# Optimization experiments

Hardware: AMD Instinct MI355X
Metric: run time of the kernel (lower is better)

## Reference

```python
import jax, jax.numpy as jnp
import numpy as np

MUL = 8              # multiplicity of 0e and 1o irreps (feature dim = MUL + 3*MUL = 32)
N_NODES = 25000
N_EDGES = 200000
EDGE_ATTR_DIM = 16
RADIAL_HIDDEN = 64
N_PATHS = 5          # CG paths: 0e*0e->0e, 0e*1o->1o, 1o*0e->1o, 1o*1o->0e, 1o*1o->1o


def _split(x):
    # x: [*, MUL + 3*MUL] -> scalars [*, MUL], vectors [*, MUL, 3]
    return x[:, :MUL], x[:, MUL:].reshape(x.shape[0], MUL, 3)


def _radial(edge_attr, W1, W2):
    # two-layer radial net (e3nn FullyConnectedNet style, silu, fan-in normalized)
    h = jax.nn.silu(edge_attr @ W1 / jnp.sqrt(float(EDGE_ATTR_DIM)))
    w = h @ W2 / jnp.sqrt(float(RADIAL_HIDDEN))
    return w.reshape(-1, N_PATHS, MUL, MUL)  # [E, 5, MUL, MUL]


def _edge_tp(xs, xv, s0, s1, w):
    # per-edge FullyConnectedTensorProduct(irreps_in, irreps_sh, irreps_out)
    # xs:[E,MUL] xv:[E,MUL,3] s0:[E] s1:[E,3] w:[E,5,MUL,MUL]
    dot = jnp.einsum('emc,ec->em', xv, s1) / jnp.sqrt(3.0)          # 1o x 1o -> 0e
    out_s = (jnp.einsum('emn,em->en', w[:, 0], xs) * s0[:, None]
             + jnp.einsum('emn,em->en', w[:, 3], dot)) / jnp.sqrt(2.0 * MUL)
    cross = jnp.cross(xv, s1[:, None, :]) / jnp.sqrt(2.0)            # 1o x 1o -> 1o
    out_v = (jnp.einsum('emn,em->en', w[:, 1], xs)[:, :, None] * s1[:, None, :]
             + jnp.einsum('emn,emc->enc', w[:, 2], xv) * s0[:, None, None]
             + jnp.einsum('emn,emc->enc', w[:, 4], cross)) / jnp.sqrt(3.0 * MUL)
    return out_s, out_v


def setup_inputs() -> dict:
    key = jax.random.key(0)
    ks = jax.random.split(key, 12)
    node_attr = jax.random.normal(ks[0], (N_NODES, 4 * MUL), jnp.float32)
    edge_index = jax.random.randint(ks[1], (2, N_EDGES), 0, N_NODES, dtype=jnp.int32)
    edge_attr = jax.random.normal(ks[2], (N_EDGES, EDGE_ATTR_DIM), jnp.float32)
    edge_sh = jax.random.normal(ks[3], (N_EDGES, 4), jnp.float32)
    WSZ = N_PATHS * MUL * MUL
    return {
        'node_attr': node_attr,
        'edge_index': edge_index,
        'edge_attr': edge_attr,
        'edge_sh': edge_sh,
        'Wq0': jax.random.normal(ks[4], (MUL, MUL), jnp.float32),
        'Wq1': jax.random.normal(ks[5], (MUL, MUL), jnp.float32),
        'kW1': jax.random.normal(ks[6], (EDGE_ATTR_DIM, RADIAL_HIDDEN), jnp.float32),
        'kW2': jax.random.normal(ks[7], (RADIAL_HIDDEN, WSZ), jnp.float32),
        'vW1': jax.random.normal(ks[8], (EDGE_ATTR_DIM, RADIAL_HIDDEN), jnp.float32),
        'vW2': jax.random.normal(ks[9], (RADIAL_HIDDEN, WSZ), jnp.float32),
        'Wd0': jax.random.normal(ks[10], (MUL, MUL), jnp.float32),
        'Wd1': jax.random.normal(ks[11], (MUL, MUL), jnp.float32),
    }


def reference(node_attr, edge_index, edge_attr, edge_sh,
              Wq0, Wq1, kW1, kW2, vW1, vW2, Wd0, Wd1):
    src, dst = edge_index[0], edge_index[1]
    inv_sqrt_mul = 1.0 / jnp.sqrt(float(MUL))

    # q = o3.Linear(irreps_in -> irreps_query): mixes multiplicities within each irrep
    ns, nv = _split(node_attr)
    qs = ns @ Wq0 * inv_sqrt_mul                                   # [N, MUL]
    qv = jnp.einsum('nmc,mk->nkc', nv, Wq1) * inv_sqrt_mul          # [N, MUL, 3]

    # per-edge keys/values: gather src features, tensor product with edge_sh
    xs, xv = ns[src], nv[src]
    s0, s1 = edge_sh[:, 0], edge_sh[:, 1:4]
    wk = _radial(edge_attr, kW1, kW2)
    wv = _radial(edge_attr, vW1, vW2)
    ks_, kv_ = _edge_tp(xs, xv, s0, s1, wk)
    vs_, vv_ = _edge_tp(xs, xv, s0, s1, wv)

    # dot = FullyConnectedTensorProduct(query, key, '0e') per edge
    logits = (jnp.einsum('mn,em,en->e', Wd0, qs[dst], ks_)
              + jnp.einsum('mn,emc,enc->e', Wd1, qv[dst], kv_) / jnp.sqrt(3.0)
              ) / jnp.sqrt(2.0 * MUL)
    exp = jnp.exp(logits)[:, None]                                 # [E, 1]

    # scatter-mean normalization
    z_sum = jax.ops.segment_sum(exp, dst, num_segments=N_NODES)
    cnt = jax.ops.segment_sum(jnp.ones_like(exp), dst, num_segments=N_NODES)
    z = z_sum / jnp.maximum(cnt, 1.0)
    alpha = exp / z[dst]
    attn = jnp.sqrt(jax.nn.relu(alpha))

    # weighted scatter-sum aggregation
    v_edge = jnp.concatenate([vs_, vv_.reshape(-1, 3 * MUL)], axis=1)  # [E, 32]
    out = jax.ops.segment_sum(attn * v_edge, dst, num_segments=N_NODES)
    return out
```

## Files before the change

### kernel.cpp

```cpp
#include <hip/hip_runtime.h>
#include <hip/hip_bf16.h>
#include <math.h>

#define NE 200000
#define NN 25000

static constexpr float INV_SQRT3  = 0.5773502691896258f;
static constexpr float INV_SQRT2  = 0.7071067811865476f;
static constexpr float INV_SQRT8  = 0.3535533905932738f;
static constexpr float INV_SQRT24 = 0.2041241452319315f;

typedef __attribute__((ext_vector_type(8))) short bf16x8;
typedef __attribute__((ext_vector_type(4))) float f32x4;

union U16x8 { uint4 u; bf16x8 v; };

__device__ __forceinline__ unsigned f2bf1(float f) {
  unsigned u = __float_as_uint(f);
  return (u + 0x7FFFu + ((u >> 16) & 1u)) >> 16;
}
__device__ __forceinline__ unsigned packbf(float a, float b) {
  union { __hip_bfloat162 h; unsigned u; } c;
  c.h = __float22bfloat162_rn(make_float2(a, b));
  return c.u;
}
__device__ __forceinline__ float bflo(unsigned u) { return __uint_as_float(u << 16); }
__device__ __forceinline__ float bfhi(unsigned u) { return __uint_as_float(u & 0xFFFF0000u); }

__global__ __launch_bounds__(256) void prep_kernel(
    const float* __restrict__ kW1, const float* __restrict__ kW2,
    const float* __restrict__ vW1, const float* __restrict__ vW2,
    const float* __restrict__ node_attr,
    const float* __restrict__ Wq0, const float* __restrict__ Wq1,
    const float* __restrict__ Wd0, const float* __restrict__ Wd1,
    const int*   __restrict__ edge_index,
    unsigned short* __restrict__ afrag,
    unsigned short* __restrict__ afrag1,
    float* __restrict__ qd, float* __restrict__ qvd,
    int* __restrict__ hist)
{
  int t = blockIdx.x * blockDim.x + threadIdx.x;
  if (t < 4096) {
    int j    = t & 7;
    int lane = (t >> 3) & 63;
    int rt   = (t >> 9) & 3;
    int b    = (t >> 11) & 1;
    int quad = lane >> 4;
    int k    = quad * 8 + j;
    int jeff = k & 15;
    int r    = rt * 16 + (lane & 15);
    const float* W = b ? vW1 : kW1;
    afrag1[t] = (unsigned short)f2bf1(W[jeff * 64 + r]);
  }
  if (t < 40960) {
    int j    = t & 7;
    int lane = (t >> 3) & 63;
    int kk   = (t >> 9) & 1;
    int ot   = (t >> 10) & 1;
    int ci   = t >> 11;
    int b    = ci / 10;
    int rem  = ci - b * 10;
    int p    = rem >> 1;
    int hf   = rem & 1;
    int r    = kk * 32 + ((lane >> 4) << 3) + j;
    int o    = p * 64 + hf * 32 + ot * 16 + (lane & 15);
    const float* W = b ? vW2 : kW2;
    afrag[t] = (unsigned short)f2bf1(W[r * 320 + o]);
  }
#pragma unroll
  for (int i = 0; i < 5; ++i) {
    int e = t * 5 + i;
    if (e < NE) atomicAdd(&hist[edge_index[NE + e]], 1);
  }
  if (t < NN) {
    int n = t;
    float ns[8], nv[24];
#pragma unroll
    for (int i = 0; i < 8; ++i)  ns[i] = node_attr[n * 32 + i];
#pragma unroll
    for (int i = 0; i < 24; ++i) nv[i] = node_attr[n * 32 + 8 + i];
    float qs[8];
#pragma unroll
    for (int m = 0; m < 8; ++m) {
      float a = 0.f;
#pragma unroll
      for (int i = 0; i < 8; ++i) a = fmaf(ns[i], Wq0[i * 8 + m], a);
      qs[m] = a * INV_SQRT8;
    }
#pragma unroll
    for (int k = 0; k < 8; ++k) {
      float a = 0.f;
#pragma unroll
      for (int m = 0; m < 8; ++m) a = fmaf(qs[m], Wd0[m * 8 + k], a);
      qd[n * 8 + k] = a;
    }
    float qv[24];
#pragma unroll
    for (int k = 0; k < 8; ++k) {
#pragma unroll
      for (int c = 0; c < 3; ++c) {
        float a = 0.f;
#pragma unroll
        for (int m = 0; m < 8; ++m) a = fmaf(nv[m * 3 + c], Wq1[m * 8 + k], a);
        qv[k * 3 + c] = a * INV_SQRT8;
      }
    }
#pragma unroll
    for (int k = 0; k < 8; ++k) {
#pragma unroll
      for (int c = 0; c < 3; ++c) {
        float a = 0.f;
#pragma unroll
        for (int m = 0; m < 8; ++m) a = fmaf(qv[m * 3 + c], Wd1[m * 8 + k], a);
        qvd[n * 24 + k * 3 + c] = a;
      }
    }
  }
}

__global__ __launch_bounds__(1024) void scan_kernel(
    const int* __restrict__ hist, int* __restrict__ off, int* __restrict__ cursor)
{
  __shared__ int wsum[16];
  const int tid  = threadIdx.x;
  const int lane = tid & 63;
  const int wv   = tid >> 6;
  const int base = tid * 25;
  int loc[25];
  int s = 0;
#pragma unroll
  for (int i = 0; i < 25; ++i) {
    int idx = base + i;
    int v = (idx < NN) ? hist[idx] : 0;
    loc[i] = s;
    s += v;
  }
  int incl = s;
#pragma unroll
  for (int d = 1; d < 64; d <<= 1) {
    int t = __shfl_up(incl, d, 64);
    if (lane >= d) incl += t;
  }
  int wexcl = incl - s;
  if (lane == 63) wsum[wv] = incl;
  __syncthreads();
  if (wv == 0 && lane < 16) {
    int v = wsum[lane];
    int inc2 = v;
#pragma unroll
    for (int d = 1; d < 16; d <<= 1) {
      int t = __shfl_up(inc2, d, 64);
      if (lane >= d) inc2 += t;
    }
    wsum[lane] = inc2 - v;
  }
  __syncthreads();
  int tbase = wsum[wv] + wexcl;
#pragma unroll
  for (int i = 0; i < 25; ++i) {
    int idx = base + i;
    if (idx < NN) { int e = tbase + loc[i]; off[idx] = e; cursor[idx] = e; }
  }
  if (tid == 1023) off[NN] = tbase + s;
}

__global__ __launch_bounds__(64) void edge_kernel(
    const float* __restrict__ node_attr,
    const int*   __restrict__ edge_index,
    const float* __restrict__ edge_attr,
    const float* __restrict__ edge_sh,
    const unsigned short* __restrict__ afrag1,
    const unsigned short* __restrict__ afrag,
    const float* __restrict__ qd,   const float* __restrict__ qvd,
    int* __restrict__ cursor,
    float* __restrict__ exo, float* __restrict__ wout)
{
  __shared__ unsigned char smem[9216];
  const int lane = threadIdx.x;
  const int l15  = lane & 15;
  const int quad = lane >> 4;
  unsigned char* sea = smem;
  unsigned char* sh  = smem;
  unsigned char* swp = smem;

  const int e = blockIdx.x * 64 + lane;
  const bool valid = (e < NE);
  const int el  = valid ? e : (NE - 1);
  const int src = edge_index[el];
  const int dst = edge_index[NE + el];

  int pos = 0;
  if (valid) pos = atomicAdd(&cursor[dst], 1);

  const float s0  = edge_sh[el * 4 + 0];
  const float s1x = edge_sh[el * 4 + 1];
  const float s1y = edge_sh[el * 4 + 2];
  const float s1z = edge_sh[el * 4 + 3];

  {
    float ea[16];
    const float4* ea4 = (const float4*)(edge_attr + (size_t)el * 16);
#pragma unroll
    for (int i = 0; i < 4; ++i) {
      float4 v = ea4[i];
      ea[4*i+0] = v.x; ea[4*i+1] = v.y; ea[4*i+2] = v.z; ea[4*i+3] = v.w;
    }
    unsigned char* myrow = sea + lane * 80;
    unsigned hi[8];
    float lo[16];
#pragma unroll
    for (int i = 0; i < 8; ++i) {
      unsigned pk = packbf(ea[2*i], ea[2*i+1]);
      hi[i] = pk;
      lo[2*i]   = ea[2*i]   - bflo(pk);
      lo[2*i+1] = ea[2*i+1] - bfhi(pk);
    }
    uint4 w0 = {hi[0], hi[1], hi[2], hi[3]};
    uint4 w1 = {hi[4], hi[5], hi[6], hi[7]};
    *(uint4*)(myrow)      = w0;
    *(uint4*)(myrow + 16) = w1;
    uint4 w2, w3;
    w2.x = packbf(lo[0], lo[1]);   w2.y = packbf(lo[2], lo[3]);
    w2.z = packbf(lo[4], lo[5]);   w2.w = packbf(lo[6], lo[7]);
    w3.x = packbf(lo[8], lo[9]);   w3.y = packbf(lo[10], lo[11]);
    w3.z = packbf(lo[12], lo[13]); w3.w = packbf(lo[14], lo[15]);
    *(uint4*)(myrow + 32) = w2;
    *(uint4*)(myrow + 48) = w3;
  }

  U16x8 B1[4];
#pragma unroll
  for (int et = 0; et < 4; ++et)
    B1[et].u = *(const uint4*)(sea + (et*16 + l15) * 80 + quad * 16);

  float xs[8], xv[8][3];
  {
    const float4* na4 = (const float4*)(node_attr + (size_t)src * 32);
    float tmp[32];
#pragma unroll
    for (int i = 0; i < 8; ++i) {
      float4 v = na4[i];
      tmp[4*i+0] = v.x; tmp[4*i+1] = v.y; tmp[4*i+2] = v.z; tmp[4*i+3] = v.w;
    }
#pragma unroll
    for (int m = 0; m < 8; ++m) xs[m] = tmp[m];
#pragma unroll
    for (int m = 0; m < 8; ++m) {
      xv[m][0] = tmp[8 + 3*m + 0];
      xv[m][1] = tmp[8 + 3*m + 1];
      xv[m][2] = tmp[8 + 3*m + 2];
    }
  }

  const uint4* AF  = (const uint4*)afrag;
  const uint4* AF1 = (const uint4*)afrag1;
  float ex = 0.f;

#pragma unroll 1
  for (int b = 0; b < 2; ++b) {
#pragma unroll 1
    for (int rt = 0; rt < 4; ++rt) {
      U16x8 a1;
      a1.u = AF1[(b * 4 + rt) * 64 + lane];
#pragma unroll
      for (int et = 0; et < 4; ++et) {
        f32x4 c = {0.f, 0.f, 0.f, 0.f};
        c = __builtin_amdgcn_mfma_f32_16x16x32_bf16(a1.v, B1[et].v, c, 0, 0, 0);
        float hh[4];
#pragma unroll
        for (int i = 0; i < 4; ++i) {
          float x = c[i] * 0.25f;
          hh[i] = x / (1.f + __expf(-x));
        }
        uint2 pk;
        pk.x = packbf(hh[0], hh[1]);
        pk.y = packbf(hh[2], hh[3]);
        *(uint2*)(sh + (et*16 + l15) * 144 + (rt*16 + quad*4) * 2) = pk;
      }
    }

    bf16x8 B[4][2];
#pragma unroll
    for (int et = 0; et < 4; ++et) {
#pragma unroll
      for (int kk = 0; kk < 2; ++kk) {
        U16x8 cv;
        cv.u = *(const uint4*)(sh + (et*16 + l15) * 144 + kk * 64 + quad * 16);
        B[et][kk] = cv.v;
      }
    }

    float accs[8];
    float accv[8][3];
#pragma unroll
    for (int n = 0; n < 8; ++n) {
      accs[n] = 0.f;
      accv[n][0] = 0.f; accv[n][1] = 0.f; accv[n][2] = 0.f;
    }

#pragma unroll 1
    for (int cc = 0; cc < 10; ++cc) {
      const int p  = cc >> 1;
      const int hf = cc & 1;
      const int ci = b * 10 + cc;
      U16x8 a00, a01, a10, a11;
      a00.u = AF[(ci*4 + 0) * 64 + lane];
      a01.u = AF[(ci*4 + 1) * 64 + lane];
      a10.u = AF[(ci*4 + 2) * 64 + lane];
      a11.u = AF[(ci*4 + 3) * 64 + lane];

#pragma unroll
      for (int et = 0; et < 4; ++et) {
        f32x4 c0 = {0.f, 0.f, 0.f, 0.f};
        f32x4 c1 = {0.f, 0.f, 0.f, 0.f};
        c0 = __builtin_amdgcn_mfma_f32_16x16x32_bf16(a00.v, B[et][0], c0, 0, 0, 0);
        c0 = __builtin_amdgcn_mfma_f32_16x16x32_bf16(a01.v, B[et][1], c0, 0, 0, 0);
        c1 = __builtin_amdgcn_mfma_f32_16x16x32_bf16(a10.v, B[et][0], c1, 0, 0, 0);
        c1 = __builtin_amdgcn_mfma_f32_16x16x32_bf16(a11.v, B[et][1], c1, 0, 0, 0);
        unsigned char* wrow = swp + (et*16 + l15) * 80;
        uint2 p0; p0.x = packbf(c0.x, c0.y); p0.y = packbf(c0.z, c0.w);
        uint2 p1; p1.x = packbf(c1.x, c1.y); p1.y = packbf(c1.z, c1.w);
        *(uint2*)(wrow + quad * 8)      = p0;
        *(uint2*)(wrow + 32 + quad * 8) = p1;
      }

      const uint4* wr = (const uint4*)(swp + (size_t)lane * 80);
#pragma unroll
      for (int h2 = 0; h2 < 2; ++h2) {
        uint4 qa = wr[h2 * 2], qb = wr[h2 * 2 + 1];
        float wvv[16];
        {
          unsigned qs_[8] = {qa.x,qa.y,qa.z,qa.w, qb.x,qb.y,qb.z,qb.w};
#pragma unroll
          for (int i = 0; i < 8; ++i) {
            wvv[2*i]   = bflo(qs_[i]);
            wvv[2*i+1] = bfhi(qs_[i]);
          }
        }
#pragma unroll
        for (int mm = 0; mm < 2; ++mm) {
          const int m = hf * 4 + h2 * 2 + mm;
          const float* wm = &wvv[mm * 8];
          if (p == 0) {
            float g = xs[m] * s0;
#pragma unroll
            for (int n = 0; n < 8; ++n) accs[n] = fmaf(wm[n], g, accs[n]);
          } else if (p == 1) {
            float a = xs[m];
            float gx = a * s1x, gy = a * s1y, gz = a * s1z;
#pragma unroll
            for (int n = 0; n < 8; ++n) {
              accv[n][0] = fmaf(wm[n], gx, accv[n][0]);
              accv[n][1] = fmaf(wm[n], gy, accv[n][1]);
              accv[n][2] = fmaf(wm[n], gz, accv[n][2]);
            }
          } else if (p == 2) {
            float gx = xv[m][0] * s0, gy = xv[m][1] * s0, gz = xv[m][2] * s0;
#pragma unroll
            for (int n = 0; n < 8; ++n) {
              accv[n][0] = fmaf(wm[n], gx, accv[n][0]);
              accv[n][1] = fmaf(wm[n], gy, accv[n][1]);
              accv[n][2] = fmaf(wm[n], gz, accv[n][2]);
            }
          } else if (p == 3) {
            float dm = (xv[m][0]*s1x + xv[m][1]*s1y + xv[m][2]*s1z) * INV_SQRT3;
#pragma unroll
            for (int n = 0; n < 8; ++n) accs[n] = fmaf(wm[n], dm, accs[n]);
          } else {
            float crx = (xv[m][1]*s1z - xv[m][2]*s1y) * INV_SQRT2;
            float cry = (xv[m][2]*s1x - xv[m][0]*s1z) * INV_SQRT2;
            float crz = (xv[m][0]*s1y - xv[m][1]*s1x) * INV_SQRT2;
#pragma unroll
            for (int n = 0; n < 8; ++n) {
              accv[n][0] = fmaf(wm[n], crx, accv[n][0]);
              accv[n][1] = fmaf(wm[n], cry, accv[n][1]);
              accv[n][2] = fmaf(wm[n], crz, accv[n][2]);
            }
          }
        }
      }
    }

    if (b == 0) {
      float lg = 0.f, lv = 0.f;
#pragma unroll
      for (int n = 0; n < 8; ++n) lg = fmaf(accs[n], qd[dst * 8 + n], lg);
#pragma unroll
      for (int n = 0; n < 8; ++n) {
#pragma unroll
        for (int c = 0; c < 3; ++c)
          lv = fmaf(accv[n][c], qvd[dst * 24 + n * 3 + c], lv);
      }
      float logit = (lg * (1.f / 32.f) +
                     lv * (0.125f * INV_SQRT24) * INV_SQRT3) * 0.25f;
      ex = __expf(logit);
      if (valid) exo[pos] = ex;
    } else {
      if (valid) {
        float a = sqrtf(ex);
        const float ss = a * (1.f / 32.f);
        const float sv = a * (0.125f * INV_SQRT24);
        float4* v4 = (float4*)(wout + (size_t)pos * 32);
        float4 o;
        o.x = accs[0] * ss; o.y = accs[1] * ss;
        o.z = accs[2] * ss; o.w = accs[3] * ss;
        v4[0] = o;
        o.x = accs[4] * ss; o.y = accs[5] * ss;
        o.z = accs[6] * ss; o.w = accs[7] * ss;
        v4[1] = o;
        o.x = accv[0][0] * sv; o.y = accv[0][1] * sv;
        o.z = accv[0][2] * sv; o.w = accv[1][0] * sv;
        v4[2] = o;
        o.x = accv[1][1] * sv; o.y = accv[1][2] * sv;
        o.z = accv[2][0] * sv; o.w = accv[2][1] * sv;
        v4[3] = o;
        o.x = accv[2][2] * sv; o.y = accv[3][0] * sv;
        o.z = accv[3][1] * sv; o.w = accv[3][2] * sv;
        v4[4] = o;
        o.x = accv[4][0] * sv; o.y = accv[4][1] * sv;
        o.z = accv[4][2] * sv; o.w = accv[5][0] * sv;
        v4[5] = o;
        o.x = accv[5][1] * sv; o.y = accv[5][2] * sv;
        o.z = accv[6][0] * sv; o.w = accv[6][1] * sv;
        v4[6] = o;
        o.x = accv[6][2] * sv; o.y = accv[7][0] * sv;
        o.z = accv[7][1] * sv; o.w = accv[7][2] * sv;
        v4[7] = o;
      }
    }
  }
}

__global__ __launch_bounds__(256) void gather_kernel(
    const int* __restrict__ off,
    const float* __restrict__ exo,
    const float* __restrict__ wout,
    float* __restrict__ out)
{
  const int tid  = threadIdx.x;
  const int wave = tid >> 6;
  const int lane = tid & 63;
  const int n = blockIdx.x * 4 + wave;
  if (n >= NN) return;
  const int start = off[n];
  const int end   = off[n + 1];
  const int cnt   = end - start;

  float zp = 0.f;
  for (int j = start + lane; j < end; j += 64) zp += exo[j];
#pragma unroll
  for (int s = 32; s >= 1; s >>= 1) zp += __shfl_xor(zp, s, 64);

  const int q  = lane & 7;
  const int rr = lane >> 3;
  float4 acc = {0.f, 0.f, 0.f, 0.f};
  const float4* w4 = (const float4*)wout;
  for (int j = start + rr; j < end; j += 8) {
    float4 v = w4[(size_t)j * 8 + q];
    acc.x += v.x; acc.y += v.y; acc.z += v.z; acc.w += v.w;
  }
#pragma unroll
  for (int s = 8; s < 64; s <<= 1) {
    acc.x += __shfl_xor(acc.x, s, 64);
    acc.y += __shfl_xor(acc.y, s, 64);
    acc.z += __shfl_xor(acc.z, s, 64);
    acc.w += __shfl_xor(acc.w, s, 64);
  }
  if (rr == 0) {
    float s = (cnt > 0 && zp > 0.f) ? sqrtf((float)cnt / zp) : 0.f;
    float4 o = {acc.x * s, acc.y * s, acc.z * s, acc.w * s};
    ((float4*)out)[(size_t)n * 8 + q] = o;
  }
}

extern "C" void kernel_launch(void* const* d_in, const int* in_sizes, int n_in,
                              void* d_out, int out_size, void* d_ws, size_t ws_size,
                              hipStream_t stream)
{
  const float* node_attr  = (const float*)d_in[0];
  const int*   edge_index = (const int*)  d_in[1];
  const float* edge_attr  = (const float*)d_in[2];
  const float* edge_sh    = (const float*)d_in[3];
  const float* Wq0 = (const float*)d_in[4];
  const float* Wq1 = (const float*)d_in[5];
  const float* kW1 = (const float*)d_in[6];
  const float* kW2 = (const float*)d_in[7];
  const float* vW1 = (const float*)d_in[8];
  const float* vW2 = (const float*)d_in[9];
  const float* Wd0 = (const float*)d_in[10];
  const float* Wd1 = (const float*)d_in[11];
  float* out = (float*)d_out;

  float* ws = (float*)d_ws;
  float* qd     = ws;
  float* qvd    = qd   + 200000;
  unsigned short* afrag  = (unsigned short*)(qvd + 600000);
  unsigned short* afrag1 = afrag + 40960;
  int* hist   = (int*)(afrag1 + 4096);
  int* off    = hist + 25024;
  int* cursor = off  + 25056;
  float* exo  = (float*)(cursor + 25024);
  float* wout = exo + 200000;

  hipMemsetAsync(hist, 0, 25024 * sizeof(int), stream);

  prep_kernel<<<160, 256, 0, stream>>>(
      kW1, kW2, vW1, vW2, node_attr, Wq0, Wq1, Wd0, Wd1, edge_index,
      afrag, afrag1, qd, qvd, hist);
  scan_kernel<<<1, 1024, 0, stream>>>(hist, off, cursor);
  edge_kernel<<<(NE + 63) / 64, 64, 0, stream>>>(
      node_attr, edge_index, edge_attr, edge_sh,
      afrag1, afrag, qd, qvd, cursor, exo, wout);
  gather_kernel<<<(NN + 3) / 4, 256, 0, stream>>>(off, exo, wout, out);
}
```

Before: 238.7 us.

## Keep radial weights fp32 in LDS, vectorize scan, split prep kernel work

The edge kernel now writes the MFMA accumulator outputs to shared memory as fp32 with a 144-byte row stride. This replaces packing them to bf16 and unpacking after the readback, removing conversion ALU work at the cost of more LDS traffic. The scan kernel reads 32 histogram entries per thread with int4 loads instead of 25 scalar loads. The prep kernel gives node-query work its own thread range, separate from the weight-fragment and histogram threads, and its grid grows to cover both ranges.

```diff
diff --git a/kernel.cpp b/kernel.cpp
--- a/kernel.cpp
+++ b/kernel.cpp
@@ -66,14 +66,15 @@
     int o    = p * 64 + hf * 32 + ot * 16 + (lane & 15);
     const float* W = b ? vW2 : kW2;
     afrag[t] = (unsigned short)f2bf1(W[r * 320 + o]);
-  }
-#pragma unroll
-  for (int i = 0; i < 5; ++i) {
-    int e = t * 5 + i;
-    if (e < NE) atomicAdd(&hist[edge_index[NE + e]], 1);
-  }
-  if (t < NN) {
-    int n = t;
+#pragma unroll
+    for (int i = 0; i < 5; ++i) {
+      int e = t * 5 + i;
+      if (e < NE) atomicAdd(&hist[edge_index[NE + e]], 1);
+    }
+  }
+  int tn = t - 40960;
+  if (tn >= 0 && tn < NN) {
+    int n = tn;
     float ns[8], nv[24];
 #pragma unroll
     for (int i = 0; i < 8; ++i)  ns[i] = node_attr[n * 32 + i];
@@ -125,15 +126,22 @@
   const int tid  = threadIdx.x;
   const int lane = tid & 63;
   const int wv   = tid >> 6;
-  const int base = tid * 25;
-  int loc[25];
+  const int base = tid * 32;
+  int loc[32];
   int s = 0;
-#pragma unroll
-  for (int i = 0; i < 25; ++i) {
-    int idx = base + i;
-    int v = (idx < NN) ? hist[idx] : 0;
-    loc[i] = s;
-    s += v;
+  if (base < NN) {
+    const int4* h4 = (const int4*)(hist + base);
+#pragma unroll
+    for (int q = 0; q < 8; ++q) {
+      int4 v4 = h4[q];
+      loc[4*q+0] = s; s += v4.x;
+      loc[4*q+1] = s; s += v4.y;
+      loc[4*q+2] = s; s += v4.z;
+      loc[4*q+3] = s; s += v4.w;
+    }
+  } else {
+#pragma unroll
+    for (int i = 0; i < 32; ++i) loc[i] = 0;
   }
   int incl = s;
 #pragma unroll
@@ -156,10 +164,12 @@
   }
   __syncthreads();
   int tbase = wsum[wv] + wexcl;
-#pragma unroll
-  for (int i = 0; i < 25; ++i) {
-    int idx = base + i;
-    if (idx < NN) { int e = tbase + loc[i]; off[idx] = e; cursor[idx] = e; }
+  if (base < NN) {
+#pragma unroll
+    for (int i = 0; i < 32; ++i) {
+      int idx = base + i;
+      if (idx < NN) { int e2 = tbase + loc[i]; off[idx] = e2; cursor[idx] = e2; }
+    }
   }
   if (tid == 1023) off[NN] = tbase + s;
 }
@@ -317,26 +327,18 @@
         c0 = __builtin_amdgcn_mfma_f32_16x16x32_bf16(a01.v, B[et][1], c0, 0, 0, 0);
         c1 = __builtin_amdgcn_mfma_f32_16x16x32_bf16(a10.v, B[et][0], c1, 0, 0, 0);
         c1 = __builtin_amdgcn_mfma_f32_16x16x32_bf16(a11.v, B[et][1], c1, 0, 0, 0);
-        unsigned char* wrow = swp + (et*16 + l15) * 80;
-        uint2 p0; p0.x = packbf(c0.x, c0.y); p0.y = packbf(c0.z, c0.w);
-        uint2 p1; p1.x = packbf(c1.x, c1.y); p1.y = packbf(c1.z, c1.w);
-        *(uint2*)(wrow + quad * 8)      = p0;
-        *(uint2*)(wrow + 32 + quad * 8) = p1;
-      }
-
-      const uint4* wr = (const uint4*)(swp + (size_t)lane * 80);
+        unsigned char* wrow = swp + (et*16 + l15) * 144;
+        *(f32x4*)(wrow + quad * 16)      = c0;
+        *(f32x4*)(wrow + 64 + quad * 16) = c1;
+      }
+
+      const float4* wr = (const float4*)(swp + (size_t)lane * 144);
 #pragma unroll
       for (int h2 = 0; h2 < 2; ++h2) {
-        uint4 qa = wr[h2 * 2], qb = wr[h2 * 2 + 1];
-        float wvv[16];
-        {
-          unsigned qs_[8] = {qa.x,qa.y,qa.z,qa.w, qb.x,qb.y,qb.z,qb.w};
-#pragma unroll
-          for (int i = 0; i < 8; ++i) {
-            wvv[2*i]   = bflo(qs_[i]);
-            wvv[2*i+1] = bfhi(qs_[i]);
-          }
-        }
+        float4 qa = wr[h2*4+0], qb = wr[h2*4+1];
+        float4 qc = wr[h2*4+2], qd2 = wr[h2*4+3];
+        float wvv[16] = {qa.x,qa.y,qa.z,qa.w, qb.x,qb.y,qb.z,qb.w,
+                         qc.x,qc.y,qc.z,qc.w, qd2.x,qd2.y,qd2.z,qd2.w};
 #pragma unroll
         for (int mm = 0; mm < 2; ++mm) {
           const int m = hf * 4 + h2 * 2 + mm;
@@ -504,7 +506,7 @@
 
   hipMemsetAsync(hist, 0, 25024 * sizeof(int), stream);
 
-  prep_kernel<<<160, 256, 0, stream>>>(
+  prep_kernel<<<259, 256, 0, stream>>>(
       kW1, kW2, vW1, vW2, node_attr, Wq0, Wq1, Wd0, Wd1, edge_index,
       afrag, afrag1, qd, qvd, hist);
   scan_kernel<<<1, 1024, 0, stream>>>(hist, off, cursor);
```

After: 220.7 us. -7.5%, faster.
